# Optimization experiments

Hardware: AMD Instinct MI355X
Metric: run time of the kernel (lower is better)

## Reference

```python
import jax, jax.numpy as jnp
import numpy as np

T, B, H = 512, 32, 512   # seq, batch, hidden_dim (hidden has 2*H channels)
D = 512                  # label_dim
V = 32000                # vocab
L = 2048                 # number of labels (spans)
K = 2                    # tags per label (regularized ragged tags)


def setup_inputs() -> dict:
    key = jax.random.key(0)
    ks = jax.random.split(key, 11)
    hidden = jax.random.normal(ks[0], (T, B, 2 * H), dtype=jnp.float32)
    begins = jax.random.randint(ks[1], (L,), 1, T - 1)   # begin-1 >= 0
    ends = jax.random.randint(ks[2], (L,), 1, T - 1)     # end <= T-1, end-1 >= 0
    bids = jax.random.randint(ks[3], (L,), 0, B)
    tags = jax.random.randint(ks[4], (L, K), 0, V)
    s = 1.0 / np.sqrt(2 * H)
    Wc = jax.random.uniform(ks[5], (D, 2 * H), minval=-s, maxval=s, dtype=jnp.float32)
    bc = jax.random.uniform(ks[6], (D,), minval=-s, maxval=s, dtype=jnp.float32)
    Wp = jax.random.uniform(ks[7], (D, 2 * H), minval=-s, maxval=s, dtype=jnp.float32)
    bp = jax.random.uniform(ks[8], (D,), minval=-s, maxval=s, dtype=jnp.float32)
    s2 = 1.0 / np.sqrt(D)
    Wo = jax.random.uniform(ks[9], (V, D), minval=-s2, maxval=s2, dtype=jnp.float32)
    bo = jnp.zeros((V,), jnp.float32)
    # discard probs per SoftmaxLoss._discard_probs from synthetic counts
    counts = jax.random.uniform(ks[10], (V,), minval=0.5, maxval=100.0, dtype=jnp.float32)
    freqs = counts / counts.sum()
    discard_probs = jnp.maximum(1.0 - jnp.sqrt(1e-4 / freqs), 0.0)
    return dict(hidden=hidden, Wc=Wc, bc=bc, Wp=Wp, bp=bp, Wo=Wo, bo=bo,
                discard_probs=discard_probs, begins=begins, ends=ends,
                bids=bids, tags=tags)


def reference(hidden, Wc, bc, Wp, bp, Wo, bo, discard_probs,
              begins, ends, bids, tags):
    Hd = hidden.shape[-1] // 2
    # span gathers (vectorized over all labels)
    h_bm1 = hidden[begins - 1, bids]                 # [L, 2H]
    h_end = hidden[ends, bids]                       # [L, 2H]
    context = jnp.concatenate([h_bm1[:, :Hd], h_end[:, Hd:]], axis=-1)  # [L, 2H]
    phrase = (hidden[begins, bids] + hidden[ends - 1, bids]) * 0.5      # [L, 2H]
    # FFNs (dropout = identity in eval mode)
    cf = jnp.tanh(context @ Wc.T + bc)               # [L, D]
    pf = jnp.tanh(phrase @ Wp.T + bp)                # [L, D]
    feats = jnp.concatenate([cf, pf], axis=0)        # [2L, D]
    # softmax loss with discard-prob scaling
    logsm = jax.nn.log_softmax(feats @ Wo.T + bo, axis=-1)  # [2L, V]
    tg = jnp.concatenate([tags, tags], axis=0)       # [2L, K]
    neg = -jnp.take_along_axis(logsm, tg, axis=-1)   # [2L, K]
    ratio = 1.0 - discard_probs[tg]                  # [2L, K]
    loss_rows = (neg * ratio).sum(-1) / ratio.sum(-1)  # [2L]
    n = tg.shape[0]
    return (loss_rows.sum() / (n + 1e-5)).reshape(1)
```

## Files before the change

kernel.cpp:

```cpp
#include <hip/hip_runtime.h>
#include <stdint.h>

typedef uint16_t u16;
typedef uint8_t  u8;
typedef __bf16 bf16x8 __attribute__((ext_vector_type(8)));
typedef float f32x4 __attribute__((ext_vector_type(4)));
typedef int i32x4 __attribute__((ext_vector_type(4)));
typedef int i32x8 __attribute__((ext_vector_type(8)));

#define NSC    8
#define NTILES 250
#define NPART  32
#define NROWS  4096

__device__ __forceinline__ u16 f2b(float x) {
    uint32_t u = __float_as_uint(x);
    u += 0x7FFF + ((u >> 16) & 1);
    return (u16)(u >> 16);
}

__device__ __forceinline__ u8 f32_to_fp8(float x) {
    uint32_t sign = (__float_as_uint(x) >> 24) & 0x80;
    float ax = fminf(fabsf(x), 448.f);
    uint32_t r;
    if (ax < 0.015625f) {
        r = (uint32_t)(int)rintf(ax * 512.f);
    } else {
        uint32_t u = __float_as_uint(ax);
        u += 0x0007FFFF + ((u >> 20) & 1);
        r = (((u >> 23) - 120) << 3) | ((u >> 20) & 7);
    }
    return (u8)(sign | r);
}

__device__ __forceinline__ float fp8_val(int b) {
    int e = (b >> 3) & 0xF, m = b & 7;
    float v = e ? __uint_as_float((uint32_t)(((e + 120) << 23) | (m << 20)))
                : (float)m * 0.001953125f;
    return (b & 0x80) ? -v : v;
}

__device__ __forceinline__ void cp16(const void* g, void* l) {
    __builtin_amdgcn_global_load_lds(
        (const __attribute__((address_space(1))) uint32_t*)g,
        (__attribute__((address_space(3))) uint32_t*)l, 16, 0, 0);
}

__device__ __forceinline__ float fast_tanh(float x) {
    x = fminf(15.f, fmaxf(-15.f, x));
    float e = __expf(2.f * x);
    return (e - 1.f) / (e + 1.f);
}

__global__ void k_prep(const float* __restrict__ Wc, const float* __restrict__ Wp,
                       const float* __restrict__ hidden, const int* __restrict__ begins,
                       const int* __restrict__ ends, const int* __restrict__ bids,
                       const float* __restrict__ Wo, u8* __restrict__ Wo8,
                       u16* __restrict__ Wc_b, u16* __restrict__ Wp_b,
                       u16* __restrict__ ctx, u16* __restrict__ phr) {
    int b = blockIdx.x;
    if (b >= 2304) {
        int i = ((b - 2304) * 256 + threadIdx.x) * 4;
        const int stride = 2048 * 256 * 4;
        for (; i < 16384000; i += stride) {
            float4 v = *(const float4*)(Wo + i);
            u8 o[4] = {f32_to_fp8(v.x * 32.f), f32_to_fp8(v.y * 32.f),
                       f32_to_fp8(v.z * 32.f), f32_to_fp8(v.w * 32.f)};
            *(uint32_t*)(Wo8 + i) = *(const uint32_t*)o;
        }
        return;
    }
    if (b < 256) {
        int i = b * 2048 + threadIdx.x * 8;
        float4 a0 = *(const float4*)(Wc + i), a1 = *(const float4*)(Wc + i + 4);
        float4 p0 = *(const float4*)(Wp + i), p1 = *(const float4*)(Wp + i + 4);
        u16 oc[8] = {f2b(a0.x), f2b(a0.y), f2b(a0.z), f2b(a0.w),
                     f2b(a1.x), f2b(a1.y), f2b(a1.z), f2b(a1.w)};
        u16 op[8] = {f2b(p0.x), f2b(p0.y), f2b(p0.z), f2b(p0.w),
                     f2b(p1.x), f2b(p1.y), f2b(p1.z), f2b(p1.w)};
        *(int4*)(Wc_b + i) = *(const int4*)oc;
        *(int4*)(Wp_b + i) = *(const int4*)op;
        return;
    }
    int l = b - 256;
    int bg = begins[l], e = ends[l], bd = bids[l];
    const float* h_bm1 = hidden + ((size_t)(bg - 1) * 32 + bd) * 1024;
    const float* h_e   = hidden + ((size_t)e * 32 + bd) * 1024;
    const float* h_b   = hidden + ((size_t)bg * 32 + bd) * 1024;
    const float* h_em1 = hidden + ((size_t)(e - 1) * 32 + bd) * 1024;
    int d = threadIdx.x * 4;
    float4 c4 = (d < 512) ? *(const float4*)(h_bm1 + d) : *(const float4*)(h_e + d);
    float4 b4 = *(const float4*)(h_b + d);
    float4 e4 = *(const float4*)(h_em1 + d);
    u16 co[4] = {f2b(c4.x), f2b(c4.y), f2b(c4.z), f2b(c4.w)};
    u16 po[4] = {f2b(0.5f * (b4.x + e4.x)), f2b(0.5f * (b4.y + e4.y)),
                 f2b(0.5f * (b4.z + e4.z)), f2b(0.5f * (b4.w + e4.w))};
    *(uint64_t*)(ctx + (size_t)l * 1024 + d) = *(const uint64_t*)co;
    *(uint64_t*)(phr + (size_t)l * 1024 + d) = *(const uint64_t*)po;
}

__global__ __launch_bounds__(256) void k_feats(const u16* __restrict__ ctx, const u16* __restrict__ phr,
        const u16* __restrict__ Wc, const u16* __restrict__ Wp,
        const float* __restrict__ bc, const float* __restrict__ bp,
        u8* __restrict__ feats) {
    __shared__ __align__(16) u16 lA[64 * 32];
    __shared__ __align__(16) u16 lB[64 * 32];
    int z = blockIdx.z;
    const u16* A = z ? phr : ctx;
    const u16* W = z ? Wp : Wc;
    const float* bias = z ? bp : bc;
    int m0 = blockIdx.x * 64;
    int n0 = blockIdx.y * 64;
    int t = threadIdx.x;
    int lane = t & 63, w = t >> 6;
    int lrow = lane & 15, lq = lane >> 4;
    f32x4 zero = {0.f, 0.f, 0.f, 0.f};
    f32x4 acc[4];
    for (int i = 0; i < 4; i++) acc[i] = zero;
    int row = t >> 2, kseg = (t & 3) * 8;
    for (int kt = 0; kt < 32; kt++) {
        int k0 = kt * 32;
        __syncthreads();
        cp16(&A[(size_t)(m0 + row) * 1024 + k0 + kseg], &lA[t * 8]);
        cp16(&W[(size_t)(n0 + row) * 1024 + k0 + kseg], &lB[t * 8]);
        __syncthreads();
        bf16x8 af = *(bf16x8*)&lA[(w * 16 + lrow) * 32 + lq * 8];
        for (int ns = 0; ns < 4; ns++) {
            bf16x8 bfr = *(bf16x8*)&lB[(ns * 16 + lrow) * 32 + lq * 8];
            acc[ns] = __builtin_amdgcn_mfma_f32_16x16x32_bf16(af, bfr, acc[ns], 0, 0, 0);
        }
    }
    int zbase = z * 2048;
    for (int ns = 0; ns < 4; ns++) {
        int col = n0 + ns * 16 + lrow;
        float bv = bias[col];
        for (int r = 0; r < 4; r++) {
            int orow = zbase + m0 + w * 16 + lq * 4 + r;
            feats[(size_t)orow * 512 + col] = f32_to_fp8(16.f * fast_tanh(acc[ns][r] + bv));
        }
    }
}

__global__ __launch_bounds__(512, 1) void k_lse(const u8* __restrict__ feats,
        const u8* __restrict__ Wo, const float* __restrict__ bo, float* __restrict__ ps) {
    __shared__ __align__(16) u8 lds[4][128 * 128];
    int m0 = blockIdx.x * 128;
    int sc = blockIdx.y;
    int ts = (NTILES * sc) / NSC, te = (NTILES * (sc + 1)) / NSC;
    int t = threadIdx.x;
    int lane = t & 63, w = t >> 6;
    int lrow = lane & 15, lq = lane >> 4;
    int wrow = (w & 1) * 64, wcol = (w >> 1) * 32;
    int xm = lrow & 7;
    int xoA = ((2 * lq) ^ xm) * 16;
    int xoB = ((2 * lq + 1) ^ xm) * 16;

    int srow = t >> 3;
    int kb = ((t & 7) ^ ((t >> 3) & 7)) * 16;

    auto stageB = [&](int slot, int gr) {
        const u8* pB = Wo + (size_t)((gr >> 2) * 128 + srow) * 512 + (gr & 3) * 128 + kb;
        cp16(pB, &lds[slot][t * 16]);
        cp16(pB + (size_t)64 * 512, &lds[slot][t * 16 + 8192]);
    };

    int gr0 = ts * 4;
    stageB(0, gr0);
    stageB(1, gr0 + 1);
    stageB(2, gr0 + 2);

    i32x8 af[4][4];
#pragma unroll
    for (int mi = 0; mi < 4; mi++) {
        const u8* pa = feats + (size_t)(m0 + wrow + mi * 16 + lrow) * 512 + lq * 32;
#pragma unroll
        for (int kc = 0; kc < 4; kc++) {
            i32x4 lo = *(const i32x4*)(pa + kc * 128);
            i32x4 hi = *(const i32x4*)(pa + kc * 128 + 16);
            af[mi][kc] = __builtin_shufflevector(lo, hi, 0, 1, 2, 3, 4, 5, 6, 7);
        }
    }

    float s_state[4][4];
    for (int mi = 0; mi < 4; mi++)
        for (int r = 0; r < 4; r++) s_state[mi][r] = 0.f;
    f32x4 zero = {0.f, 0.f, 0.f, 0.f};
    f32x4 acc[4][2];
    const float inv512 = 1.f / 512.f;

    for (int tile = ts; tile < te; ++tile) {
        int grt = tile * 4;
        bool notlast = (tile + 1 < te);
#pragma unroll
        for (int mi = 0; mi < 4; mi++)
#pragma unroll
            for (int ni = 0; ni < 2; ni++) acc[mi][ni] = zero;
#pragma unroll
        for (int kc = 0; kc < 4; kc++) {
            if (notlast || kc < 2)
                asm volatile("s_waitcnt vmcnt(4)" ::: "memory");
            else if (kc == 2)
                asm volatile("s_waitcnt vmcnt(2)" ::: "memory");
            else
                asm volatile("s_waitcnt vmcnt(0)" ::: "memory");
            __builtin_amdgcn_s_barrier();
            if (notlast || kc == 0)
                stageB((kc + 3) & 3, grt + kc + 3);
            const u8* bufB = lds[kc];
            __builtin_amdgcn_s_setprio(1);
#pragma unroll
            for (int ni = 0; ni < 2; ni++) {
                const u8* pb = bufB + (wcol + ni * 16 + lrow) * 128;
                i32x4 blo = *(const i32x4*)(pb + xoA);
                i32x4 bhi = *(const i32x4*)(pb + xoB);
                i32x8 bfr = __builtin_shufflevector(blo, bhi, 0, 1, 2, 3, 4, 5, 6, 7);
#pragma unroll
                for (int mi = 0; mi < 4; mi++)
                    acc[mi][ni] = __builtin_amdgcn_mfma_scale_f32_16x16x128_f8f6f4(
                        af[mi][kc], bfr, acc[mi][ni], 0, 0,
                        0, 0x7F7F7F7F, 0, 0x7F7F7F7F);
            }
            __builtin_amdgcn_s_setprio(0);
        }
        int n0 = tile * 128;
#pragma unroll
        for (int ni = 0; ni < 2; ni++) {
            float bv = bo[n0 + wcol + ni * 16 + lrow];
#pragma unroll
            for (int mi = 0; mi < 4; mi++)
#pragma unroll
                for (int r = 0; r < 4; r++)
                    s_state[mi][r] += __expf(fmaf(acc[mi][ni][r], inv512, bv));
        }
    }
    for (int mi = 0; mi < 4; mi++)
    for (int r = 0; r < 4; r++) {
        float s = s_state[mi][r];
        for (int off = 1; off < 16; off <<= 1) s += __shfl_xor(s, off);
        if (lrow == 0) {
            int row = m0 + wrow + mi * 16 + lq * 4 + r;
            ps[row * NPART + sc * 4 + (w >> 1)] = s;
        }
    }
}

__global__ void k_taglog(const u8* __restrict__ feats, const u8* __restrict__ Wo,
        const float* __restrict__ bo, const int* __restrict__ tags, float* __restrict__ tlog) {
    int i = blockIdx.x * 4 + (threadIdx.x >> 6);
    int lane = threadIdx.x & 63;
    int t0 = tags[(i & 2047) * 2 + 0];
    int t1 = tags[(i & 2047) * 2 + 1];
    uint64_t fa = *(const uint64_t*)(feats + (size_t)i * 512 + lane * 8);
    uint64_t wa = *(const uint64_t*)(Wo + (size_t)t0 * 512 + lane * 8);
    uint64_t wb = *(const uint64_t*)(Wo + (size_t)t1 * 512 + lane * 8);
    float s0 = 0.f, s1 = 0.f;
    for (int j = 0; j < 8; j++) {
        float fv = fp8_val((int)((fa >> (8 * j)) & 0xFF));
        s0 += fv * fp8_val((int)((wa >> (8 * j)) & 0xFF));
        s1 += fv * fp8_val((int)((wb >> (8 * j)) & 0xFF));
    }
    for (int off = 32; off >= 1; off >>= 1) {
        s0 += __shfl_down(s0, off);
        s1 += __shfl_down(s1, off);
    }
    if (lane == 0) {
        tlog[i * 2 + 0] = s0 * (1.f / 512.f) + bo[t0];
        tlog[i * 2 + 1] = s1 * (1.f / 512.f) + bo[t1];
    }
}

__global__ void k_final(const float* __restrict__ ps,
        const float* __restrict__ tlog, const int* __restrict__ tags,
        const float* __restrict__ dp, float* __restrict__ out) {
    __shared__ float red[256];
    int i = blockIdx.x * 256 + threadIdx.x;
    float S = 0.f;
    for (int j = 0; j < NPART; j++) S += ps[i * NPART + j];
    float lse = logf(S);
    float num = 0.f, den = 0.f;
    for (int k = 0; k < 2; k++) {
        int tg = tags[(i & 2047) * 2 + k];
        float r = 1.0f - dp[tg];
        num += r * (lse - tlog[i * 2 + k]);
        den += r;
    }
    red[threadIdx.x] = num / den;
    __syncthreads();
    for (int s = 128; s > 0; s >>= 1) {
        if (threadIdx.x < s) red[threadIdx.x] += red[threadIdx.x + s];
        __syncthreads();
    }
    if (threadIdx.x == 0) atomicAdd(out, red[0] / (4096.0f + 1e-5f));
}

extern "C" void kernel_launch(void* const* d_in, const int* in_sizes, int n_in,
                              void* d_out, int out_size, void* d_ws, size_t ws_size,
                              hipStream_t stream) {
    const float* hidden = (const float*)d_in[0];
    const float* Wc     = (const float*)d_in[1];
    const float* bc     = (const float*)d_in[2];
    const float* Wp     = (const float*)d_in[3];
    const float* bp     = (const float*)d_in[4];
    const float* Wo     = (const float*)d_in[5];
    const float* bo     = (const float*)d_in[6];
    const float* dp     = (const float*)d_in[7];
    const int* begins   = (const int*)d_in[8];
    const int* ends     = (const int*)d_in[9];
    const int* bids     = (const int*)d_in[10];
    const int* tags     = (const int*)d_in[11];
    float* out = (float*)d_out;

    u8*  Wo8     = (u8*)d_ws;
    u16* Wc_b    = (u16*)((char*)d_ws + 16384000);
    u16* Wp_b    = Wc_b + 524288;
    u16* ctx_b   = Wp_b + 524288;
    u16* phr_b   = ctx_b + 2097152;
    u8*  feats8  = (u8*)(phr_b + 2097152);
    float* ps    = (float*)ctx_b;
    float* tlog  = ps + NROWS * NPART;

    k_prep<<<4352, 256, 0, stream>>>(Wc, Wp, hidden, begins, ends, bids,
                                     Wo, Wo8, Wc_b, Wp_b, ctx_b, phr_b);
    k_feats<<<dim3(32, 8, 2), 256, 0, stream>>>(ctx_b, phr_b, Wc_b, Wp_b, bc, bp, feats8);
    k_lse<<<dim3(32, NSC), 512, 0, stream>>>(feats8, Wo8, bo, ps);
    k_taglog<<<1024, 256, 0, stream>>>(feats8, Wo8, bo, tags, tlog);
    hipMemsetAsync(d_out, 0, sizeof(float), stream);
    k_final<<<16, 256, 0, stream>>>(ps, tlog, tags, dp, out);
}
```

Baseline: 270.4 us.

## Software-pipeline softmax exp epilogue with next tile's MFMA chain

Holds the previous tile's accumulators in a second register set and spreads their exp-sum across the four k-chunks of the next tile, so the transcendental work can interleave with the MFMAs instead of running as a serialized epilogue. The scale and log2(e) are folded into a single constant so each element costs one fma plus exp2f. The bias load is moved into the first k-chunk to hide its latency. This needs 32 more VGPRs for the pending accumulators, which may lower occupancy or cause spills, and the initial -1e30 bias makes the first pass add exp2 of a very negative number, which should contribute zero.

```diff
diff --git a/kernel.cpp b/kernel.cpp
--- a/kernel.cpp
+++ b/kernel.cpp
@@ -181,12 +181,20 @@
         }
     }
 
+    const float C1 = 0.0028177637517362567f;
+    const float L2E = 1.4426950408889634f;
     float s_state[4][4];
     for (int mi = 0; mi < 4; mi++)
         for (int r = 0; r < 4; r++) s_state[mi][r] = 0.f;
     f32x4 zero = {0.f, 0.f, 0.f, 0.f};
     f32x4 acc[4][2];
-    const float inv512 = 1.f / 512.f;
+    f32x4 pacc[4][2];
+#pragma unroll
+    for (int mi = 0; mi < 4; mi++)
+#pragma unroll
+        for (int ni = 0; ni < 2; ni++) pacc[mi][ni] = zero;
+    float pbv0 = -1e30f, pbv1 = -1e30f;
+    float nbv0 = 0.f, nbv1 = 0.f;
 
     for (int tile = ts; tile < te; ++tile) {
         int grt = tile * 4;
@@ -206,6 +214,11 @@
             __builtin_amdgcn_s_barrier();
             if (notlast || kc == 0)
                 stageB((kc + 3) & 3, grt + kc + 3);
+            if (kc == 0) {
+                int n0c = tile * 128 + wcol + lrow;
+                nbv0 = bo[n0c];
+                nbv1 = bo[n0c + 16];
+            }
             const u8* bufB = lds[kc];
             __builtin_amdgcn_s_setprio(1);
 #pragma unroll
@@ -221,18 +234,27 @@
                         0, 0x7F7F7F7F, 0, 0x7F7F7F7F);
             }
             __builtin_amdgcn_s_setprio(0);
-        }
-        int n0 = tile * 128;
-#pragma unroll
-        for (int ni = 0; ni < 2; ni++) {
-            float bv = bo[n0 + wcol + ni * 16 + lrow];
-#pragma unroll
-            for (int mi = 0; mi < 4; mi++)
-#pragma unroll
-                for (int r = 0; r < 4; r++)
-                    s_state[mi][r] += __expf(fmaf(acc[mi][ni][r], inv512, bv));
-        }
-    }
+#pragma unroll
+            for (int r = 0; r < 4; r++)
+                s_state[kc][r] += exp2f(fmaf(pacc[kc][0][r], C1, pbv0));
+#pragma unroll
+            for (int r = 0; r < 4; r++)
+                s_state[kc][r] += exp2f(fmaf(pacc[kc][1][r], C1, pbv1));
+        }
+#pragma unroll
+        for (int mi = 0; mi < 4; mi++)
+#pragma unroll
+            for (int ni = 0; ni < 2; ni++) pacc[mi][ni] = acc[mi][ni];
+        pbv0 = nbv0 * L2E;
+        pbv1 = nbv1 * L2E;
+    }
+#pragma unroll
+    for (int mi = 0; mi < 4; mi++)
+#pragma unroll
+        for (int r = 0; r < 4; r++) {
+            s_state[mi][r] += exp2f(fmaf(pacc[mi][0][r], C1, pbv0));
+            s_state[mi][r] += exp2f(fmaf(pacc[mi][1][r], C1, pbv1));
+        }
     for (int mi = 0; mi < 4; mi++)
     for (int r = 0; r < 4; r++) {
         float s = s_state[mi][r];
```

Result: slower. 284.9 us (+5.3%).
